# Optimization experiments

Measured on AMD Instinct MI355X. Metric: run time of the kernel, lower is better.

The kernel has to match this reference:

```python
import jax, jax.numpy as jnp
import numpy as np

B, S, D = 4, 4096, 64
TEMPERATURE = 8.0  # sqrt(64), matching Dense(64) projections in source


def setup_inputs() -> dict:
    key = jax.random.key(0)
    kq, kk, kv = jax.random.split(key, 3)
    q = jax.random.normal(kq, (B, S, D), dtype=jnp.float32)
    k = jax.random.normal(kk, (B, S, D), dtype=jnp.float32)
    v = jax.random.normal(kv, (B, S, D), dtype=jnp.float32)
    return {"q": q, "k": k, "v": v}


def reference(q, k, v):
    # attn = softmax(QK^T / temperature); dropout is identity at inference
    scores = jnp.einsum("bqd,bkd->bqk", q, k) / TEMPERATURE  # [B,S,S]
    attn = jax.nn.softmax(scores, axis=-1)
    out = jnp.einsum("bqk,bkd->bqd", attn, v)  # [B,S,D]
    return (out, attn)
```

## Files before the change

kernel.cpp:

```cpp
#include <hip/hip_runtime.h>
#include <cstddef>

namespace {
constexpr int kB = 4;
constexpr int kS = 4096;
constexpr int kD = 64;
constexpr float kC = 0.18033688011112042f;

typedef float  f32x4  __attribute__((ext_vector_type(4)));
typedef __bf16 bf16x8 __attribute__((ext_vector_type(8)));
typedef short  s16x2  __attribute__((ext_vector_type(2)));
typedef short  s16x4  __attribute__((ext_vector_type(4)));
typedef short  s16x8  __attribute__((ext_vector_type(8)));

constexpr size_t kWsQ = (size_t)kB * kS * kD;
constexpr size_t kWsNeed = 3 * kWsQ * sizeof(short);
}

__device__ __forceinline__ s16x2 pack_bf16(float a, float b) {
    __bf16 ha = (__bf16)a, hb = (__bf16)b;
    s16x2 r;
    r.x = __builtin_bit_cast(short, ha);
    r.y = __builtin_bit_cast(short, hb);
    return r;
}

__global__ __launch_bounds__(256)
void prepass_kernel(const float* __restrict__ q, const float* __restrict__ k,
                    const float* __restrict__ v, short* __restrict__ qb,
                    short* __restrict__ kb, short* __restrict__ vt)
{
    __shared__ float lt[64][65];
    const int bid = blockIdx.x, tid = threadIdx.x;
    if (bid < 512) {
        const float* src = (bid < 256) ? q : k;
        short* dst = (bid < 256) ? qb : kb;
        const int base = (bid & 255) * 4096;
        #pragma unroll
        for (int c = 0; c < 4; ++c) {
            const int idx = base + c * 1024 + tid * 4;
            float4 f = *(const float4*)(src + idx);
            s16x4 o = __builtin_shufflevector(pack_bf16(f.x, f.y), pack_bf16(f.z, f.w), 0, 1, 2, 3);
            *(s16x4*)(dst + idx) = o;
        }
    } else {
        const int vb = bid - 512;
        const int b = vb >> 6, j0 = (vb & 63) * 64;
        const int r = tid >> 2, seg = tid & 3;
        const float* vrow = v + ((size_t)(b * kS) + j0 + r) * kD + seg * 16;
        #pragma unroll
        for (int u = 0; u < 4; ++u) {
            float4 f = *(const float4*)(vrow + 4 * u);
            lt[r][seg * 16 + 4 * u + 0] = f.x;
            lt[r][seg * 16 + 4 * u + 1] = f.y;
            lt[r][seg * 16 + 4 * u + 2] = f.z;
            lt[r][seg * 16 + 4 * u + 3] = f.w;
        }
        __syncthreads();
        const int d = r, js = seg * 16;
        short* drow = vt + ((size_t)(b * kD) + d) * kS + j0 + js;
        #pragma unroll
        for (int w = 0; w < 4; ++w) {
            s16x4 o = __builtin_shufflevector(
                pack_bf16(lt[js + 4 * w + 0][d], lt[js + 4 * w + 1][d]),
                pack_bf16(lt[js + 4 * w + 2][d], lt[js + 4 * w + 3][d]), 0, 1, 2, 3);
            *(s16x4*)(drow + 4 * w) = o;
        }
    }
}

__global__ __launch_bounds__(128)
void attn_mfma_kernel(const short* __restrict__ qb, const short* __restrict__ kb,
                      const short* __restrict__ vt, float* __restrict__ outg,
                      float* __restrict__ attng)
{
    __shared__ __align__(16) short Pl[2][2][16][36];
    __shared__ float lds_out[16][68];
    __shared__ float lds_rs[16];
    __shared__ float lds_linv[16];

    const int b  = blockIdx.x >> 8;
    const int i0 = (blockIdx.x & 255) * 16;
    const int lane = threadIdx.x & 63;
    const int wave = threadIdx.x >> 6;
    const int t = lane & 15;
    const int q = lane >> 4;

    const short* Qb = qb + ((size_t)(b * kS) + i0) * kD;
    const short* Kb = kb + (size_t)(b * kS) * kD;
    const short* Vt = vt + (size_t)b * kD * kS;

    const bf16x8 qf0 = *(const bf16x8*)(Qb + t * kD + 8 * q);
    const bf16x8 qf1 = *(const bf16x8*)(Qb + t * kD + 32 + 8 * q);

    const int jbeg = wave * (kS / 2);
    const int jend = jbeg + (kS / 2);

    f32x4 oacc[4];
    #pragma unroll
    for (int dt = 0; dt < 4; ++dt) oacc[dt] = (f32x4){0.f, 0.f, 0.f, 0.f};
    float rs = 0.f;

    int buf = 0;
    for (int j0 = jbeg; j0 < jend; j0 += 32) {
        #pragma unroll
        for (int h = 0; h < 2; ++h) {
            const short* p = Kb + (j0 + 16 * h + t) * kD + 8 * q;
            const bf16x8 ka0 = *(const bf16x8*)p;
            const bf16x8 ka1 = *(const bf16x8*)(p + 32);
            f32x4 acc = (f32x4){0.f, 0.f, 0.f, 0.f};
            acc = __builtin_amdgcn_mfma_f32_16x16x32_bf16(ka0, qf0, acc, 0, 0, 0);
            acc = __builtin_amdgcn_mfma_f32_16x16x32_bf16(ka1, qf1, acc, 0, 0, 0);
            const float e0 = __builtin_amdgcn_exp2f(acc[0] * kC);
            const float e1 = __builtin_amdgcn_exp2f(acc[1] * kC);
            const float e2 = __builtin_amdgcn_exp2f(acc[2] * kC);
            const float e3 = __builtin_amdgcn_exp2f(acc[3] * kC);
            rs += (e0 + e1) + (e2 + e3);
            const s16x4 pk = __builtin_shufflevector(pack_bf16(e0, e1), pack_bf16(e2, e3), 0, 1, 2, 3);
            *(s16x4*)&Pl[buf][wave][t][16 * h + 4 * q] = pk;
        }
        __syncthreads();

        const s16x4 lo = *(const s16x4*)&Pl[buf][wave][t][8 * q];
        const s16x4 hi = *(const s16x4*)&Pl[buf][wave][t][8 * q + 4];
        const s16x8 pw = __builtin_shufflevector(lo, hi, 0, 1, 2, 3, 4, 5, 6, 7);
        const bf16x8 pa = __builtin_bit_cast(bf16x8, pw);

        #pragma unroll
        for (int dt = 0; dt < 4; ++dt) {
            const bf16x8 vb = *(const bf16x8*)(Vt + (16 * dt + t) * kS + j0 + 8 * q);
            oacc[dt] = __builtin_amdgcn_mfma_f32_16x16x32_bf16(pa, vb, oacc[dt], 0, 0, 0);
        }
        buf ^= 1;
    }

    rs += __shfl_xor(rs, 16);
    rs += __shfl_xor(rs, 32);

    if (wave == 1) {
        #pragma unroll
        for (int dt = 0; dt < 4; ++dt)
            #pragma unroll
            for (int r = 0; r < 4; ++r)
                lds_out[4 * q + r][16 * dt + t] = oacc[dt][r];
        if (q == 0) lds_rs[t] = rs;
    }
    __syncthreads();
    if (wave == 0) {
        #pragma unroll
        for (int dt = 0; dt < 4; ++dt)
            #pragma unroll
            for (int r = 0; r < 4; ++r)
                oacc[dt][r] += lds_out[4 * q + r][16 * dt + t];
        rs += lds_rs[t];
        if (q == 0) lds_linv[t] = 1.0f / rs;
    }
    __syncthreads();

    if (wave == 0) {
        #pragma unroll
        for (int r = 0; r < 4; ++r) {
            const float li = lds_linv[4 * q + r];
            float* orow = outg + ((size_t)(b * kS) + i0 + 4 * q + r) * kD + t;
            #pragma unroll
            for (int dt = 0; dt < 4; ++dt)
                orow[16 * dt] = oacc[dt][r] * li;
        }
    }
    const float li_t = lds_linv[t];

    float* arow = attng + ((size_t)(b * kS) + i0 + t) * kS;
    for (int j0 = jbeg; j0 < jend; j0 += 16) {
        const short* p = Kb + (j0 + t) * kD + 8 * q;
        const bf16x8 ka0 = *(const bf16x8*)p;
        const bf16x8 ka1 = *(const bf16x8*)(p + 32);
        f32x4 acc = (f32x4){0.f, 0.f, 0.f, 0.f};
        acc = __builtin_amdgcn_mfma_f32_16x16x32_bf16(ka0, qf0, acc, 0, 0, 0);
        acc = __builtin_amdgcn_mfma_f32_16x16x32_bf16(ka1, qf1, acc, 0, 0, 0);
        f32x4 o;
        o[0] = __builtin_amdgcn_exp2f(acc[0] * kC) * li_t;
        o[1] = __builtin_amdgcn_exp2f(acc[1] * kC) * li_t;
        o[2] = __builtin_amdgcn_exp2f(acc[2] * kC) * li_t;
        o[3] = __builtin_amdgcn_exp2f(acc[3] * kC) * li_t;
        *(f32x4*)(arow + j0 + 4 * q) = o;
    }
}

namespace fb {
constexpr int QT = 64, JT = 64;
constexpr float kScale = 0.125f;
constexpr int LP = kD + 4;
}
__global__ __launch_bounds__(256, 1)
void attn_fp32_kernel(const float* __restrict__ qg, const float* __restrict__ kg,
                      const float* __restrict__ vg, float* __restrict__ outg,
                      float* __restrict__ attng)
{
    using namespace fb;
    __shared__ float qs[QT][LP];
    __shared__ float ks[JT][LP];
    __shared__ float es[QT][JT + 4];
    __shared__ float red[QT][17];
    __shared__ float linv[QT];
    const int tid = threadIdx.x;
    const int tx = tid & 15, ty = tid >> 4;
    const int b = blockIdx.x >> 6, qt = blockIdx.x & 63, i0 = qt * QT;
    const float* qbp = qg + ((size_t)b * kS + i0) * kD;
    const float* kbase = kg + (size_t)b * kS * kD;
    const float* vbase = vg + (size_t)b * kS * kD;
    {
        const int r = tid >> 4, c4 = (tid & 15) * 4;
        #pragma unroll
        for (int m = 0; m < 4; ++m)
            *(float4*)&qs[r + 16 * m][c4] = *(const float4*)(qbp + (r + 16 * m) * kD + c4);
    }
    float oacc[4][4]; float rsv[4];
    #pragma unroll
    for (int r = 0; r < 4; ++r) { rsv[r] = 0.f; for (int c = 0; c < 4; ++c) oacc[r][c] = 0.f; }
    for (int jt = 0; jt < kS / JT; ++jt) {
        const float* kt = kbase + (size_t)(jt * JT) * kD;
        const int r = tid >> 4, c4 = (tid & 15) * 4;
        #pragma unroll
        for (int m = 0; m < 4; ++m)
            *(float4*)&ks[r + 16 * m][c4] = *(const float4*)(kt + (r + 16 * m) * kD + c4);
        __syncthreads();
        float acc[4][4] = {{0.f}};
        #pragma unroll
        for (int d4 = 0; d4 < kD / 4; ++d4) {
            float4 qa[4], kav[4];
            #pragma unroll
            for (int r2 = 0; r2 < 4; ++r2) qa[r2] = *(const float4*)&qs[ty * 4 + r2][d4 * 4];
            #pragma unroll
            for (int c = 0; c < 4; ++c) kav[c] = *(const float4*)&ks[tx * 4 + c][d4 * 4];
            #pragma unroll
            for (int r2 = 0; r2 < 4; ++r2)
                #pragma unroll
                for (int c = 0; c < 4; ++c)
                    acc[r2][c] += qa[r2].x * kav[c].x + qa[r2].y * kav[c].y
                                + qa[r2].z * kav[c].z + qa[r2].w * kav[c].w;
        }
        #pragma unroll
        for (int r2 = 0; r2 < 4; ++r2) {
            float4 e4;
            e4.x = __expf(acc[r2][0] * kScale); e4.y = __expf(acc[r2][1] * kScale);
            e4.z = __expf(acc[r2][2] * kScale); e4.w = __expf(acc[r2][3] * kScale);
            rsv[r2] += (e4.x + e4.y) + (e4.z + e4.w);
            *(float4*)&es[ty * 4 + r2][tx * 4] = e4;
        }
        __syncthreads();
        const float* vt2 = vbase + (size_t)(jt * JT) * kD;
        #pragma unroll 4
        for (int j4 = 0; j4 < JT / 4; ++j4) {
            float4 vv[4], ea[4];
            #pragma unroll
            for (int n = 0; n < 4; ++n) vv[n] = *(const float4*)(vt2 + (size_t)(j4 * 4 + n) * kD + tx * 4);
            #pragma unroll
            for (int r2 = 0; r2 < 4; ++r2) ea[r2] = *(const float4*)&es[ty * 4 + r2][j4 * 4];
            #pragma unroll
            for (int r2 = 0; r2 < 4; ++r2) {
                oacc[r2][0] += ea[r2].x * vv[0].x + ea[r2].y * vv[1].x + ea[r2].z * vv[2].x + ea[r2].w * vv[3].x;
                oacc[r2][1] += ea[r2].x * vv[0].y + ea[r2].y * vv[1].y + ea[r2].z * vv[2].y + ea[r2].w * vv[3].y;
                oacc[r2][2] += ea[r2].x * vv[0].z + ea[r2].y * vv[1].z + ea[r2].z * vv[2].z + ea[r2].w * vv[3].z;
                oacc[r2][3] += ea[r2].x * vv[0].w + ea[r2].y * vv[1].w + ea[r2].z * vv[2].w + ea[r2].w * vv[3].w;
            }
        }
        __syncthreads();
    }
    #pragma unroll
    for (int r = 0; r < 4; ++r) red[ty * 4 + r][tx] = rsv[r];
    __syncthreads();
    if (tid < QT) {
        float s = 0.f;
        #pragma unroll
        for (int t2 = 0; t2 < 16; ++t2) s += red[tid][t2];
        linv[tid] = 1.0f / s;
    }
    __syncthreads();
    {
        float* ob = outg + ((size_t)b * kS + i0) * kD;
        #pragma unroll
        for (int r = 0; r < 4; ++r) {
            const int i = ty * 4 + r; const float li = linv[i];
            float4 o4; o4.x = oacc[r][0] * li; o4.y = oacc[r][1] * li;
            o4.z = oacc[r][2] * li; o4.w = oacc[r][3] * li;
            *(float4*)(ob + (size_t)i * kD + tx * 4) = o4;
        }
    }
    float* ab = attng + ((size_t)b * kS + i0) * kS;
    for (int jt = 0; jt < kS / JT; ++jt) {
        const float* kt = kbase + (size_t)(jt * JT) * kD;
        const int r = tid >> 4, c4 = (tid & 15) * 4;
        #pragma unroll
        for (int m = 0; m < 4; ++m)
            *(float4*)&ks[r + 16 * m][c4] = *(const float4*)(kt + (r + 16 * m) * kD + c4);
        __syncthreads();
        float acc[4][4] = {{0.f}};
        #pragma unroll
        for (int d4 = 0; d4 < kD / 4; ++d4) {
            float4 qa[4], kav[4];
            #pragma unroll
            for (int r2 = 0; r2 < 4; ++r2) qa[r2] = *(const float4*)&qs[ty * 4 + r2][d4 * 4];
            #pragma unroll
            for (int c = 0; c < 4; ++c) kav[c] = *(const float4*)&ks[tx * 4 + c][d4 * 4];
            #pragma unroll
            for (int r2 = 0; r2 < 4; ++r2)
                #pragma unroll
                for (int c = 0; c < 4; ++c)
                    acc[r2][c] += qa[r2].x * kav[c].x + qa[r2].y * kav[c].y
                                + qa[r2].z * kav[c].z + qa[r2].w * kav[c].w;
        }
        #pragma unroll
        for (int r2 = 0; r2 < 4; ++r2) {
            const int i = ty * 4 + r2; const float li = linv[i];
            float4 e4;
            e4.x = __expf(acc[r2][0] * kScale) * li; e4.y = __expf(acc[r2][1] * kScale) * li;
            e4.z = __expf(acc[r2][2] * kScale) * li; e4.w = __expf(acc[r2][3] * kScale) * li;
            *(float4*)(ab + (size_t)i * kS + jt * JT + tx * 4) = e4;
        }
        __syncthreads();
    }
}

extern "C" void kernel_launch(void* const* d_in, const int* in_sizes, int n_in,
                              void* d_out, int out_size, void* d_ws, size_t ws_size,
                              hipStream_t stream) {
    const float* q = (const float*)d_in[0];
    const float* k = (const float*)d_in[1];
    const float* v = (const float*)d_in[2];
    float* out  = (float*)d_out;
    float* attn = out + (size_t)kB * kS * kD;

    if (ws_size >= kWsNeed) {
        short* qb = (short*)d_ws;
        short* kbp = qb + kWsQ;
        short* vt = kbp + kWsQ;
        prepass_kernel<<<dim3(768), 256, 0, stream>>>(q, k, v, qb, kbp, vt);
        attn_mfma_kernel<<<dim3(kB * (kS / 16)), 128, 0, stream>>>(qb, kbp, vt, out, attn);
    } else {
        attn_fp32_kernel<<<dim3(kB * (kS / 64)), 256, 0, stream>>>(q, k, v, out, attn);
    }
}
```

Before: 418.1 us.

## Split keys across 8 waves, shuffle P in registers, nontemporal attn stores

Raises the attention block from 2 to 8 waves, each covering an eighth of the key range, and reduces partial outputs and row sums across 7 waves through LDS. The per-iteration LDS staging of the probability tile and its block barrier are replaced by cross-lane shuffles that build the MFMA A operand directly. Block indices are swizzled across batches, and the large attention-matrix writes use nontemporal stores to avoid polluting cache. This trades a larger final reduction and bigger LDS footprint for more latency hiding and no barrier in the main loop.

```diff
diff --git a/kernel.cpp b/kernel.cpp
--- a/kernel.cpp
+++ b/kernel.cpp
@@ -12,6 +12,7 @@
 typedef short  s16x2  __attribute__((ext_vector_type(2)));
 typedef short  s16x4  __attribute__((ext_vector_type(4)));
 typedef short  s16x8  __attribute__((ext_vector_type(8)));
+typedef int    i32x4  __attribute__((ext_vector_type(4)));
 
 constexpr size_t kWsQ = (size_t)kB * kS * kD;
 constexpr size_t kWsNeed = 3 * kWsQ * sizeof(short);
@@ -69,18 +70,18 @@
     }
 }
 
-__global__ __launch_bounds__(128)
+__global__ __launch_bounds__(512, 8)
 void attn_mfma_kernel(const short* __restrict__ qb, const short* __restrict__ kb,
                       const short* __restrict__ vt, float* __restrict__ outg,
                       float* __restrict__ attng)
 {
-    __shared__ __align__(16) short Pl[2][2][16][36];
-    __shared__ float lds_out[16][68];
-    __shared__ float lds_rs[16];
+    __shared__ float lds_out[7][16][68];
+    __shared__ float lds_rs[8][16];
     __shared__ float lds_linv[16];
 
-    const int b  = blockIdx.x >> 8;
-    const int i0 = (blockIdx.x & 255) * 16;
+    const int swz = (blockIdx.x & 7) * 128 + (blockIdx.x >> 3);
+    const int b  = swz >> 8;
+    const int i0 = (swz & 255) * 16;
     const int lane = threadIdx.x & 63;
     const int wave = threadIdx.x >> 6;
     const int t = lane & 15;
@@ -93,19 +94,20 @@
     const bf16x8 qf0 = *(const bf16x8*)(Qb + t * kD + 8 * q);
     const bf16x8 qf1 = *(const bf16x8*)(Qb + t * kD + 32 + 8 * q);
 
-    const int jbeg = wave * (kS / 2);
-    const int jend = jbeg + (kS / 2);
+    const int jbeg = wave * (kS / 8);
+    const int jend = jbeg + (kS / 8);
+    const int sA = t + 32 * (q & 1);
 
     f32x4 oacc[4];
     #pragma unroll
     for (int dt = 0; dt < 4; ++dt) oacc[dt] = (f32x4){0.f, 0.f, 0.f, 0.f};
     float rs = 0.f;
 
-    int buf = 0;
     for (int j0 = jbeg; j0 < jend; j0 += 32) {
+        int p0 = 0, p1 = 0, p2 = 0, p3 = 0;
         #pragma unroll
         for (int h = 0; h < 2; ++h) {
-            const short* p = Kb + (j0 + 16 * h + t) * kD + 8 * q;
+            const short* p = Kb + (size_t)(j0 + 16 * h + t) * kD + 8 * q;
             const bf16x8 ka0 = *(const bf16x8*)p;
             const bf16x8 ka1 = *(const bf16x8*)(p + 32);
             f32x4 acc = (f32x4){0.f, 0.f, 0.f, 0.f};
@@ -116,44 +118,48 @@
             const float e2 = __builtin_amdgcn_exp2f(acc[2] * kC);
             const float e3 = __builtin_amdgcn_exp2f(acc[3] * kC);
             rs += (e0 + e1) + (e2 + e3);
-            const s16x4 pk = __builtin_shufflevector(pack_bf16(e0, e1), pack_bf16(e2, e3), 0, 1, 2, 3);
-            *(s16x4*)&Pl[buf][wave][t][16 * h + 4 * q] = pk;
-        }
-        __syncthreads();
-
-        const s16x4 lo = *(const s16x4*)&Pl[buf][wave][t][8 * q];
-        const s16x4 hi = *(const s16x4*)&Pl[buf][wave][t][8 * q + 4];
-        const s16x8 pw = __builtin_shufflevector(lo, hi, 0, 1, 2, 3, 4, 5, 6, 7);
-        const bf16x8 pa = __builtin_bit_cast(bf16x8, pw);
+            const int d0 = __builtin_bit_cast(int, pack_bf16(e0, e1));
+            const int d1 = __builtin_bit_cast(int, pack_bf16(e2, e3));
+            const int a0 = __shfl(d0, sA);
+            const int a1 = __shfl(d1, sA);
+            const int b0 = __shfl(d0, sA + 16);
+            const int b1 = __shfl(d1, sA + 16);
+            if ((q >> 1) == h) { p0 = a0; p1 = a1; p2 = b0; p3 = b1; }
+        }
+        const i32x4 pi = (i32x4){p0, p1, p2, p3};
+        const bf16x8 pa = __builtin_bit_cast(bf16x8, pi);
 
         #pragma unroll
         for (int dt = 0; dt < 4; ++dt) {
-            const bf16x8 vb = *(const bf16x8*)(Vt + (16 * dt + t) * kS + j0 + 8 * q);
+            const bf16x8 vb = *(const bf16x8*)(Vt + (size_t)(16 * dt + t) * kS + j0 + 8 * q);
             oacc[dt] = __builtin_amdgcn_mfma_f32_16x16x32_bf16(pa, vb, oacc[dt], 0, 0, 0);
         }
-        buf ^= 1;
     }
 
     rs += __shfl_xor(rs, 16);
     rs += __shfl_xor(rs, 32);
 
-    if (wave == 1) {
+    if (lane < 16) lds_rs[wave][t] = rs;
+    if (wave > 0) {
         #pragma unroll
         for (int dt = 0; dt < 4; ++dt)
             #pragma unroll
             for (int r = 0; r < 4; ++r)
-                lds_out[4 * q + r][16 * dt + t] = oacc[dt][r];
-        if (q == 0) lds_rs[t] = rs;
+                lds_out[wave - 1][4 * q + r][16 * dt + t] = oacc[dt][r];
     }
     __syncthreads();
     if (wave == 0) {
         #pragma unroll
-        for (int dt = 0; dt < 4; ++dt)
-            #pragma unroll
-            for (int r = 0; r < 4; ++r)
-                oacc[dt][r] += lds_out[4 * q + r][16 * dt + t];
-        rs += lds_rs[t];
-        if (q == 0) lds_linv[t] = 1.0f / rs;
+        for (int w = 0; w < 7; ++w)
+            #pragma unroll
+            for (int dt = 0; dt < 4; ++dt)
+                #pragma unroll
+                for (int r = 0; r < 4; ++r)
+                    oacc[dt][r] += lds_out[w][4 * q + r][16 * dt + t];
+        float tot = 0.f;
+        #pragma unroll
+        for (int w = 0; w < 8; ++w) tot += lds_rs[w][t];
+        if (lane < 16) lds_linv[t] = 1.0f / tot;
     }
     __syncthreads();
 
@@ -171,7 +177,7 @@
 
     float* arow = attng + ((size_t)(b * kS) + i0 + t) * kS;
     for (int j0 = jbeg; j0 < jend; j0 += 16) {
-        const short* p = Kb + (j0 + t) * kD + 8 * q;
+        const short* p = Kb + (size_t)(j0 + t) * kD + 8 * q;
         const bf16x8 ka0 = *(const bf16x8*)p;
         const bf16x8 ka1 = *(const bf16x8*)(p + 32);
         f32x4 acc = (f32x4){0.f, 0.f, 0.f, 0.f};
@@ -182,7 +188,7 @@
         o[1] = __builtin_amdgcn_exp2f(acc[1] * kC) * li_t;
         o[2] = __builtin_amdgcn_exp2f(acc[2] * kC) * li_t;
         o[3] = __builtin_amdgcn_exp2f(acc[3] * kC) * li_t;
-        *(f32x4*)(arow + j0 + 4 * q) = o;
+        __builtin_nontemporal_store(o, (f32x4*)(arow + j0 + 4 * q));
     }
 }
 
@@ -335,7 +341,7 @@
         short* kbp = qb + kWsQ;
         short* vt = kbp + kWsQ;
         prepass_kernel<<<dim3(768), 256, 0, stream>>>(q, k, v, qb, kbp, vt);
-        attn_mfma_kernel<<<dim3(kB * (kS / 16)), 128, 0, stream>>>(qb, kbp, vt, out, attn);
+        attn_mfma_kernel<<<dim3(kB * (kS / 16)), 512, 0, stream>>>(qb, kbp, vt, out, attn);
     } else {
         attn_fp32_kernel<<<dim3(kB * (kS / 64)), 256, 0, stream>>>(q, k, v, out, attn);
     }
```

New measurement: 446.8 us. 6.9% more time.
